# Kernel tuning notes

Measured on AMD Instinct MI355X. Metric: run time of the kernel, lower is better.

The kernel has to match this reference:

```python
import jax, jax.numpy as jnp
import numpy as np

I = 64    # input_size (per quaternion component)
H = 64    # hidden_size (per quaternion component)
T = 2048  # seq_len
B = 64    # batch
G = 3 * H # gate_size for QGRU


def hamilton_kernel(r, i, j, k):
    """Build the (4*In, 4*Out) real matrix of the quaternion (Hamilton) linear map,
    matching quaternion_linear: columns [r|i|j|k], each column a vstack of components."""
    return jnp.block([[r, i, j, k],
                      [-i, r, k, -j],
                      [-j, -k, r, i],
                      [-k, j, -i, r]])


def _gates(v, h):
    # v: (B, 4*3*h) laid out quaternion-major [r(3h)|i(3h)|j(3h)|k(3h)];
    # rearrange so each of the 3 gates is a contiguous quaternion vector (B, 4h).
    b = v.shape[0]
    return v.reshape(b, 4, 3, h).transpose(0, 2, 1, 3).reshape(b, 3, 4 * h)


def setup_inputs() -> dict:
    key = jax.random.key(0)
    ks = jax.random.split(key, 12)
    s_ih = 1.0 / np.sqrt(4 * I)
    s_hh = 1.0 / np.sqrt(4 * H)
    inp = {
        "x": jax.random.normal(ks[0], (T, B, 4 * I), dtype=jnp.float32),
        "hx": jnp.zeros((B, 4 * H), dtype=jnp.float32),
        "w_ih_r": jax.random.normal(ks[1], (I, G), dtype=jnp.float32) * s_ih,
        "w_ih_i": jax.random.normal(ks[2], (I, G), dtype=jnp.float32) * s_ih,
        "w_ih_j": jax.random.normal(ks[3], (I, G), dtype=jnp.float32) * s_ih,
        "w_ih_k": jax.random.normal(ks[4], (I, G), dtype=jnp.float32) * s_ih,
        "w_hh_r": jax.random.normal(ks[5], (H, G), dtype=jnp.float32) * s_hh,
        "w_hh_i": jax.random.normal(ks[6], (H, G), dtype=jnp.float32) * s_hh,
        "w_hh_j": jax.random.normal(ks[7], (H, G), dtype=jnp.float32) * s_hh,
        "w_hh_k": jax.random.normal(ks[8], (H, G), dtype=jnp.float32) * s_hh,
        "b_ih": jnp.zeros((4 * G,), dtype=jnp.float32),
        "b_hh": jnp.zeros((4 * G,), dtype=jnp.float32),
    }
    return inp


def reference(x, hx, w_ih_r, w_ih_i, w_ih_j, w_ih_k,
              w_hh_r, w_hh_i, w_hh_j, w_hh_k, b_ih, b_hh):
    h_sz = w_hh_r.shape[0]
    W_ih = hamilton_kernel(w_ih_r, w_ih_i, w_ih_j, w_ih_k)  # (4I, 4G)
    W_hh = hamilton_kernel(w_hh_r, w_hh_i, w_hh_j, w_hh_k)  # (4H, 4G)
    # Precompute all input-side gate preactivations in one big GEMM: (T,B,4G)
    gi = jnp.einsum('tbf,fg->tbg', x, W_ih) + b_ih

    def step(h, gi_t):
        gh = _gates(h @ W_hh + b_hh, h_sz)   # (B, 3, 4H)
        g = _gates(gi_t, h_sz)               # (B, 3, 4H)
        r = jax.nn.sigmoid(g[:, 0] + gh[:, 0])     # reset gate
        z = jax.nn.sigmoid(g[:, 1] + gh[:, 1])     # update (input) gate
        n = jnp.tanh(g[:, 2] + r * gh[:, 2])       # candidate
        h_new = n + z * (h - n)
        return h_new, h_new

    h_last, out = jax.lax.scan(step, hx, gi)
    return out, h_last
```

## Files before the change

kernel.cpp:

```cpp
#include <hip/hip_runtime.h>
#include <stdint.h>

#define T_SEQ 2048

typedef __attribute__((ext_vector_type(8))) short short8;
typedef __attribute__((ext_vector_type(4))) float f32x4;

__device__ __forceinline__ unsigned short f2bf(float f){
  unsigned int u = __float_as_uint(f);
  unsigned int r = u + 0x7fffu + ((u >> 16) & 1u);
  return (unsigned short)(r >> 16);
}
__device__ __forceinline__ float bf2f(unsigned short h){
  return __uint_as_float(((unsigned int)h) << 16);
}
__device__ __forceinline__ float sig_(float x){
  float e = __builtin_amdgcn_exp2f(-1.44269504089f * x);
  return __builtin_amdgcn_rcpf(1.0f + e);
}
__device__ __forceinline__ float tanh_(float x){
  float e = __builtin_amdgcn_exp2f(2.88539008178f * x);
  return 1.0f - 2.0f * __builtin_amdgcn_rcpf(1.0f + e);
}
__device__ __forceinline__ float ham_val(int qr, int qc, int kr, int nc,
    const float* wr, const float* wi, const float* wj, const float* wk){
  int cc = qr ^ qc;
  const float* w = (cc==0)?wr:(cc==1)?wi:(cc==2)?wj:wk;
  float v = w[kr*192 + nc];
  if ((0x5390u >> (qr*4+qc)) & 1u) v = -v;
  return v;
}

__global__ __launch_bounds__(256) void k_prep_bt(const float* __restrict__ wr,
    const float* __restrict__ wi, const float* __restrict__ wj,
    const float* __restrict__ wk, unsigned short* __restrict__ BT){
  int idx = blockIdx.x*256 + threadIdx.x;
  int c = idx / 768, kp = idx - c*768;
  int kk = kp & 255, piece = kp >> 8;
  int qr = kk >> 6, kr = kk & 63;
  int e = (c/48)*16 + (c & 15);
  int g = (c % 48) >> 4;
  int qc = e >> 6;
  int nc = g*64 + (e & 63);
  float v = ham_val(qr, qc, kr, nc, wr, wi, wj, wk);
  unsigned short hi = f2bf(v);
  unsigned short o = (piece == 1) ? f2bf(v - bf2f(hi)) : hi;
  BT[(size_t)c*768 + kp] = o;
}

__global__ __launch_bounds__(256) void k_prep_whh(const float* __restrict__ wr,
    const float* __restrict__ wi, const float* __restrict__ wj,
    const float* __restrict__ wk, unsigned short* __restrict__ WF){
  int idx = blockIdx.x*256 + threadIdx.x;
  int lane = idx & 63;
  int kt = (idx >> 6) & 1;
  int m  = (idx >> 7) & 3;
  int ws3 = idx >> 9;
  int w = ws3 / 3, s = ws3 - w*3;
  int quad = lane >> 4, u = lane & 15;
  int col = s*64 + w*16 + u;
  const float* mat = (m==0)?wr:(m==1)?wi:(m==2)?wj:wk;
  short8 o;
  #pragma unroll
  for (int j = 0; j < 8; j++){
    int k = kt*32 + quad*8 + j;
    o[j] = (short)f2bf(mat[k*192 + col]);
  }
  *(short8*)(WF + (size_t)idx*8) = o;
}

__global__ __launch_bounds__(256) void k_prep_bias(const float* __restrict__ bih,
    const float* __restrict__ bhh, float* __restrict__ bias){
  int c = blockIdx.x*256 + threadIdx.x;
  int e = (c/48)*16 + (c & 15);
  int g = (c % 48) >> 4;
  int n = (e >> 6)*192 + g*64 + (e & 63);
  bias[c] = bih[n] + bhh[n];
}

__global__ __launch_bounds__(256) void k_gemm_gi(const float* __restrict__ x,
    const unsigned short* __restrict__ BT, const float* __restrict__ bias,
    float* __restrict__ gi){
  __shared__ unsigned short As[128*64];
  __shared__ unsigned short Bs[128*64];
  int tid = threadIdx.x;
  int mb = blockIdx.x / 6, nb = blockIdx.x - mb*6;
  int lane = tid & 63, wid = tid >> 6;
  int quad = lane >> 4, u = lane & 15;
  int wvm = wid >> 1, wvn = wid & 1;
  int srow = tid >> 3, cb = tid & 7;
  f32x4 acc[4][4] = {};
  for (int kc = 0; kc < 12; kc++){
    bool lop = (kc >= 8);
    int kbase = (kc & 3) * 64;
    #pragma unroll
    for (int rd = 0; rd < 4; rd++){
      int m = rd*32 + srow;
      int lc = cb ^ (m & 7);
      const float* xp = x + (size_t)(mb*128 + m)*256 + kbase + lc*8;
      float4 v0 = *(const float4*)xp;
      float4 v1 = *(const float4*)(xp + 4);
      float vv[8] = {v0.x, v0.y, v0.z, v0.w, v1.x, v1.y, v1.z, v1.w};
      short8 ov;
      #pragma unroll
      for (int q = 0; q < 8; q++){
        unsigned short hi = f2bf(vv[q]);
        ov[q] = (short)(lop ? f2bf(vv[q] - bf2f(hi)) : hi);
      }
      *(short8*)&As[m*64 + cb*8] = ov;
    }
    #pragma unroll
    for (int rd = 0; rd < 4; rd++){
      int c = rd*32 + srow;
      int lc = cb ^ (c & 7);
      const unsigned short* bp = BT + (size_t)(nb*128 + c)*768 + kc*64 + lc*8;
      *(short8*)&Bs[c*64 + cb*8] = *(const short8*)bp;
    }
    __syncthreads();
    #pragma unroll
    for (int ks = 0; ks < 2; ks++){
      short8 af[4], bf[4];
      #pragma unroll
      for (int i=0;i<4;i++){
        int row = 64*wvm + 16*i + u;
        af[i] = *(const short8*)&As[row*64 + ((4*ks+quad) ^ (u & 7))*8];
      }
      #pragma unroll
      for (int j=0;j<4;j++){
        int row = 64*wvn + 16*j + u;
        bf[j] = *(const short8*)&Bs[row*64 + ((4*ks+quad) ^ (u & 7))*8];
      }
      #pragma unroll
      for (int i=0;i<4;i++)
        #pragma unroll
        for (int j=0;j<4;j++)
          acc[i][j] = __builtin_amdgcn_mfma_f32_16x16x32_bf16(af[i], bf[j], acc[i][j], 0, 0, 0);
    }
    __syncthreads();
  }
  int cb2 = nb*128 + 64*wvn;
  #pragma unroll
  for (int j=0;j<4;j++){
    float bj = bias[cb2 + 16*j + u];
    #pragma unroll
    for (int i=0;i<4;i++){
      float* gp = gi + (size_t)(mb*128 + 64*wvm + 16*i + quad*4)*768 + cb2 + 16*j + u;
      #pragma unroll
      for (int r=0;r<4;r++)
        gp[(size_t)r*768] = acc[i][j][r] + bj;
    }
  }
}

__global__ __launch_bounds__(256, 1) void k_rec(const float* __restrict__ gi,
    const short8* __restrict__ WF, const float* __restrict__ hx,
    float* __restrict__ out){
  __shared__ unsigned short hbuf[2][256];
  int tid = threadIdx.x;
  int b = blockIdx.x;
  int lane = tid & 63, w = tid >> 6;
  int quad = lane >> 4, u = lane & 15;
  short8 Bf[12][2];
  #pragma unroll
  for (int s = 0; s < 3; s++)
    #pragma unroll
    for (int m = 0; m < 4; m++)
      #pragma unroll
      for (int kt = 0; kt < 2; kt++)
        Bf[s*4+m][kt] = WF[(size_t)((((w*3+s)*4+m)*2+kt)*64 + lane)];
  int aoff = (((u & 3) ^ (u >> 2)) * 64) + quad*8;
  float sg1 = (quad & 1)              ?  1.f : -1.f;
  float sg2 = (quad==1 || quad==2)    ?  1.f : -1.f;
  float sg3 = (quad >> 1)             ?  1.f : -1.f;
  int e = quad*64 + w*16 + u;
  float h = hx[b*256 + e];
  hbuf[0][e] = f2bf(h);
  const float* gl = gi + (size_t)b*768 + (quad*4 + w)*48 + u;
  float* outp = out + (size_t)b*256 + e;
  float pf[4][3];
  #pragma unroll
  for (int j = 0; j < 4; j++){
    const float* p = gl + (size_t)j*49152;
    pf[j][0] = p[0]; pf[j][1] = p[16]; pf[j][2] = p[32];
  }
  const float* gp   = gl + (size_t)4*49152;
  const float* glast = gl + (size_t)(T_SEQ-1)*49152;
  asm volatile("s_waitcnt lgkmcnt(0)" ::: "memory");
  __builtin_amdgcn_s_barrier();
  asm volatile("" ::: "memory");
  for (int t0 = 0; t0 < T_SEQ; t0 += 4){
    #pragma unroll
    for (int j = 0; j < 4; j++){
      const unsigned short* hb = hbuf[j & 1];
      short8 a0 = *(const short8*)&hb[aoff];
      short8 a1 = *(const short8*)&hb[aoff + 32];
      f32x4 acc[12];
      #pragma unroll
      for (int sm = 0; sm < 12; sm++)
        acc[sm] = __builtin_amdgcn_mfma_f32_16x16x32_bf16(a0, Bf[sm][0],
                    (f32x4){0.f,0.f,0.f,0.f}, 0, 0, 0);
      #pragma unroll
      for (int sm = 0; sm < 12; sm++)
        acc[sm] = __builtin_amdgcn_mfma_f32_16x16x32_bf16(a1, Bf[sm][1],
                    acc[sm], 0, 0, 0);
      float o0 = acc[0][0] + sg1*acc[1][1] + sg2*acc[2][2]  + sg3*acc[3][3];
      float o1 = acc[4][0] + sg1*acc[5][1] + sg2*acc[6][2]  + sg3*acc[7][3];
      float o2 = acc[8][0] + sg1*acc[9][1] + sg2*acc[10][2] + sg3*acc[11][3];
      float r  = sig_(pf[j][0] + o0);
      float z  = sig_(pf[j][1] + o1);
      float nn = tanh_(pf[j][2] + r * o2);
      h = nn + z * (h - nn);
      int t = t0 + j;
      outp[(size_t)t * 16384] = h;
      hbuf[(j + 1) & 1][e] = f2bf(h);
      const float* pv = (gp <= glast) ? gp : glast;
      pf[j][0] = pv[0]; pf[j][1] = pv[16]; pf[j][2] = pv[32];
      gp += 49152;
      asm volatile("s_waitcnt lgkmcnt(0)" ::: "memory");
      __builtin_amdgcn_s_barrier();
      asm volatile("" ::: "memory");
    }
  }
  out[(size_t)T_SEQ * 16384 + b*256 + e] = h;
}

extern "C" void kernel_launch(void* const* d_in, const int* in_sizes, int n_in,
                              void* d_out, int out_size, void* d_ws, size_t ws_size,
                              hipStream_t stream){
  const float* x    = (const float*)d_in[0];
  const float* hx   = (const float*)d_in[1];
  const float* wihr = (const float*)d_in[2];
  const float* wihi = (const float*)d_in[3];
  const float* wihj = (const float*)d_in[4];
  const float* wihk = (const float*)d_in[5];
  const float* whhr = (const float*)d_in[6];
  const float* whhi = (const float*)d_in[7];
  const float* whhj = (const float*)d_in[8];
  const float* whhk = (const float*)d_in[9];
  const float* bih  = (const float*)d_in[10];
  const float* bhh  = (const float*)d_in[11];
  char* ws = (char*)d_ws;
  float* gi          = (float*)ws;
  unsigned short* BT = (unsigned short*)(ws + 402653184ull);
  unsigned short* WF = (unsigned short*)(ws + 403832832ull);
  float* bias        = (float*)(ws + 404226048ull);
  k_prep_bt  <<<dim3(2304), dim3(256), 0, stream>>>(wihr, wihi, wihj, wihk, BT);
  k_prep_whh <<<dim3(24),   dim3(256), 0, stream>>>(whhr, whhi, whhj, whhk, WF);
  k_prep_bias<<<dim3(3),    dim3(256), 0, stream>>>(bih, bhh, bias);
  k_gemm_gi  <<<dim3(6144), dim3(256), 0, stream>>>(x, BT, bias, gi);
  k_rec      <<<dim3(64),   dim3(256), 0, stream>>>(gi, (const short8*)WF, hx, (float*)d_out);
}
```

Baseline: 1.461 ms.

## Process two batch rows per recurrent block to interleave independent chains

The recurrent kernel now has each block advance two batch rows, A and B, at once. The MFMA chains and gate math for the two rows are interleaved, and both rows share a single barrier per timestep, so one row's latency can overlap the other's. The hidden-state LDS buffer is padded (stride 88) to reduce bank conflicts. In exchange only half as many blocks are launched, and each block does double the per-step work and uses more registers.

After: 1.998 ms. 1.37x slower.

```diff
diff --git a/kernel.cpp b/kernel.cpp
--- a/kernel.cpp
+++ b/kernel.cpp
@@ -155,9 +155,9 @@
 __global__ __launch_bounds__(256, 1) void k_rec(const float* __restrict__ gi,
     const short8* __restrict__ WF, const float* __restrict__ hx,
     float* __restrict__ out){
-  __shared__ unsigned short hbuf[2][256];
+  __shared__ unsigned short hbuf[2][2][4][88];
   int tid = threadIdx.x;
-  int b = blockIdx.x;
+  int b0 = blockIdx.x * 2;
   int lane = tid & 63, w = tid >> 6;
   int quad = lane >> 4, u = lane & 15;
   short8 Bf[12][2];
@@ -168,60 +168,99 @@
       #pragma unroll
       for (int kt = 0; kt < 2; kt++)
         Bf[s*4+m][kt] = WF[(size_t)((((w*3+s)*4+m)*2+kt)*64 + lane)];
-  int aoff = (((u & 3) ^ (u >> 2)) * 64) + quad*8;
+  int sg = (u & 3) ^ (u >> 2);
+  int abase = sg*88 + quad*8;
   float sg1 = (quad & 1)              ?  1.f : -1.f;
   float sg2 = (quad==1 || quad==2)    ?  1.f : -1.f;
   float sg3 = (quad >> 1)             ?  1.f : -1.f;
   int e = quad*64 + w*16 + u;
-  float h = hx[b*256 + e];
-  hbuf[0][e] = f2bf(h);
-  const float* gl = gi + (size_t)b*768 + (quad*4 + w)*48 + u;
-  float* outp = out + (size_t)b*256 + e;
-  float pf[4][3];
+  int wbase = quad*88 + w*16 + u;
+  unsigned short* hb = &hbuf[0][0][0][0];
+  float hA = hx[b0*256 + e];
+  float hB = hx[b0*256 + 256 + e];
+  hb[wbase]       = f2bf(hA);
+  hb[352 + wbase] = f2bf(hB);
+  const float* glA = gi + (size_t)b0*768 + (quad*4 + w)*48 + u;
+  const float* glB = glA + 768;
+  float* outA = out + (size_t)b0*256 + e;
+  float* outB = outA + 256;
+  float pfA[4][3], pfB[4][3];
   #pragma unroll
   for (int j = 0; j < 4; j++){
-    const float* p = gl + (size_t)j*49152;
-    pf[j][0] = p[0]; pf[j][1] = p[16]; pf[j][2] = p[32];
-  }
-  const float* gp   = gl + (size_t)4*49152;
-  const float* glast = gl + (size_t)(T_SEQ-1)*49152;
+    const float* pA = glA + (size_t)j*49152;
+    const float* pB = glB + (size_t)j*49152;
+    pfA[j][0]=pA[0]; pfA[j][1]=pA[16]; pfA[j][2]=pA[32];
+    pfB[j][0]=pB[0]; pfB[j][1]=pB[16]; pfB[j][2]=pB[32];
+  }
+  const float* gpA = glA + (size_t)4*49152;
+  const float* gpB = glB + (size_t)4*49152;
+  const float* glastA = glA + (size_t)(T_SEQ-1)*49152;
+  const float* glastB = glB + (size_t)(T_SEQ-1)*49152;
   asm volatile("s_waitcnt lgkmcnt(0)" ::: "memory");
   __builtin_amdgcn_s_barrier();
   asm volatile("" ::: "memory");
   for (int t0 = 0; t0 < T_SEQ; t0 += 4){
     #pragma unroll
     for (int j = 0; j < 4; j++){
-      const unsigned short* hb = hbuf[j & 1];
-      short8 a0 = *(const short8*)&hb[aoff];
-      short8 a1 = *(const short8*)&hb[aoff + 32];
-      f32x4 acc[12];
-      #pragma unroll
-      for (int sm = 0; sm < 12; sm++)
-        acc[sm] = __builtin_amdgcn_mfma_f32_16x16x32_bf16(a0, Bf[sm][0],
-                    (f32x4){0.f,0.f,0.f,0.f}, 0, 0, 0);
-      #pragma unroll
-      for (int sm = 0; sm < 12; sm++)
-        acc[sm] = __builtin_amdgcn_mfma_f32_16x16x32_bf16(a1, Bf[sm][1],
-                    acc[sm], 0, 0, 0);
-      float o0 = acc[0][0] + sg1*acc[1][1] + sg2*acc[2][2]  + sg3*acc[3][3];
-      float o1 = acc[4][0] + sg1*acc[5][1] + sg2*acc[6][2]  + sg3*acc[7][3];
-      float o2 = acc[8][0] + sg1*acc[9][1] + sg2*acc[10][2] + sg3*acc[11][3];
-      float r  = sig_(pf[j][0] + o0);
-      float z  = sig_(pf[j][1] + o1);
-      float nn = tanh_(pf[j][2] + r * o2);
-      h = nn + z * (h - nn);
+      int ph = j & 1;
+      const unsigned short* ha = hb + ph*704;
+      short8 a0A = *(const short8*)&ha[abase];
+      short8 a1A = *(const short8*)&ha[abase + 32];
+      short8 a0B = *(const short8*)&ha[352 + abase];
+      short8 a1B = *(const short8*)&ha[352 + abase + 32];
+      f32x4 accA[12], accB[12];
+      #pragma unroll
+      for (int sm = 0; sm < 12; sm++)
+        accA[sm] = __builtin_amdgcn_mfma_f32_16x16x32_bf16(a0A, Bf[sm][0],
+                     (f32x4){0.f,0.f,0.f,0.f}, 0, 0, 0);
+      #pragma unroll
+      for (int sm = 0; sm < 12; sm++)
+        accA[sm] = __builtin_amdgcn_mfma_f32_16x16x32_bf16(a1A, Bf[sm][1],
+                     accA[sm], 0, 0, 0);
+      #pragma unroll
+      for (int sm = 0; sm < 12; sm++)
+        accB[sm] = __builtin_amdgcn_mfma_f32_16x16x32_bf16(a0B, Bf[sm][0],
+                     (f32x4){0.f,0.f,0.f,0.f}, 0, 0, 0);
+      #pragma unroll
+      for (int sm = 0; sm < 12; sm++)
+        accB[sm] = __builtin_amdgcn_mfma_f32_16x16x32_bf16(a1B, Bf[sm][1],
+                     accB[sm], 0, 0, 0);
       int t = t0 + j;
-      outp[(size_t)t * 16384] = h;
-      hbuf[(j + 1) & 1][e] = f2bf(h);
-      const float* pv = (gp <= glast) ? gp : glast;
-      pf[j][0] = pv[0]; pf[j][1] = pv[16]; pf[j][2] = pv[32];
-      gp += 49152;
+      {
+        float o0 = accA[0][0] + sg1*accA[1][1] + sg2*accA[2][2]  + sg3*accA[3][3];
+        float o1 = accA[4][0] + sg1*accA[5][1] + sg2*accA[6][2]  + sg3*accA[7][3];
+        float o2 = accA[8][0] + sg1*accA[9][1] + sg2*accA[10][2] + sg3*accA[11][3];
+        float r  = sig_(pfA[j][0] + o0);
+        float z  = sig_(pfA[j][1] + o1);
+        float nn = tanh_(pfA[j][2] + r * o2);
+        hA = nn + z * (hA - nn);
+        outA[(size_t)t * 16384] = hA;
+        hb[(ph^1)*704 + wbase] = f2bf(hA);
+        const float* pv = (gpA <= glastA) ? gpA : glastA;
+        pfA[j][0] = pv[0]; pfA[j][1] = pv[16]; pfA[j][2] = pv[32];
+        gpA += 49152;
+      }
+      {
+        float o0 = accB[0][0] + sg1*accB[1][1] + sg2*accB[2][2]  + sg3*accB[3][3];
+        float o1 = accB[4][0] + sg1*accB[5][1] + sg2*accB[6][2]  + sg3*accB[7][3];
+        float o2 = accB[8][0] + sg1*accB[9][1] + sg2*accB[10][2] + sg3*accB[11][3];
+        float r  = sig_(pfB[j][0] + o0);
+        float z  = sig_(pfB[j][1] + o1);
+        float nn = tanh_(pfB[j][2] + r * o2);
+        hB = nn + z * (hB - nn);
+        outB[(size_t)t * 16384] = hB;
+        hb[(ph^1)*704 + 352 + wbase] = f2bf(hB);
+        const float* pv = (gpB <= glastB) ? gpB : glastB;
+        pfB[j][0] = pv[0]; pfB[j][1] = pv[16]; pfB[j][2] = pv[32];
+        gpB += 49152;
+      }
       asm volatile("s_waitcnt lgkmcnt(0)" ::: "memory");
       __builtin_amdgcn_s_barrier();
       asm volatile("" ::: "memory");
     }
   }
-  out[(size_t)T_SEQ * 16384 + b*256 + e] = h;
+  out[(size_t)T_SEQ * 16384 + b0*256 + e] = hA;
+  out[(size_t)T_SEQ * 16384 + b0*256 + 256 + e] = hB;
 }
 
 extern "C" void kernel_launch(void* const* d_in, const int* in_sizes, int n_in,
@@ -248,5 +287,5 @@
   k_prep_whh <<<dim3(24),   dim3(256), 0, stream>>>(whhr, whhi, whhj, whhk, WF);
   k_prep_bias<<<dim3(3),    dim3(256), 0, stream>>>(bih, bhh, bias);
   k_gemm_gi  <<<dim3(6144), dim3(256), 0, stream>>>(x, BT, bias, gi);
-  k_rec      <<<dim3(64),   dim3(256), 0, stream>>>(gi, (const short8*)WF, hx, (float*)d_out);
-}
+  k_rec      <<<dim3(32),   dim3(256), 0, stream>>>(gi, (const short8*)WF, hx, (float*)d_out);
+}
```

## Swizzle h LDS buffer, reorder MFMAs and defer output stores in recurrence

Applied to the files above, without the earlier changes.

Applies an XOR swizzle to the bf16 hidden-state LDS buffer so the A-fragment reads and the per-thread writes avoid bank conflicts. The output store for the previous step and the prefetch of gate inputs move to the top of each step so they sit off the critical path. The reset-gate MFMAs are issued first so its sigmoid can overlap the remaining MFMAs. The software bf16 rounding is replaced with the hardware v_cvt_pk_bf16_f32 instruction. Together these target the serial per-timestep latency, at the cost of more complex indexing and inline assembly.

New measurement: 1.518 ms. +3.9%, slower.

```diff
diff --git a/kernel.cpp b/kernel.cpp
--- a/kernel.cpp
+++ b/kernel.cpp
@@ -168,13 +168,16 @@
       #pragma unroll
       for (int kt = 0; kt < 2; kt++)
         Bf[s*4+m][kt] = WF[(size_t)((((w*3+s)*4+m)*2+kt)*64 + lane)];
-  int aoff = (((u & 3) ^ (u >> 2)) * 64) + quad*8;
+  int sg = (u & 3) ^ (u >> 2);
+  int a0off = sg*64 + ((quad ^ (2*sg)) & 7)*8;
+  int a1off = sg*64 + (((quad + 4) ^ (2*sg)) & 7)*8;
   float sg1 = (quad & 1)              ?  1.f : -1.f;
   float sg2 = (quad==1 || quad==2)    ?  1.f : -1.f;
   float sg3 = (quad >> 1)             ?  1.f : -1.f;
   int e = quad*64 + w*16 + u;
+  int wboff = quad*64 + (((w*2 + (u>>3)) ^ (2*quad)) & 7)*8 + (u & 7);
   float h = hx[b*256 + e];
-  hbuf[0][e] = f2bf(h);
+  hbuf[0][wboff] = f2bf(h);
   const float* gl = gi + (size_t)b*768 + (quad*4 + w)*48 + u;
   float* outp = out + (size_t)b*256 + e;
   float pf[4][3];
@@ -183,7 +186,7 @@
     const float* p = gl + (size_t)j*49152;
     pf[j][0] = p[0]; pf[j][1] = p[16]; pf[j][2] = p[32];
   }
-  const float* gp   = gl + (size_t)4*49152;
+  const float* gp    = gl + (size_t)4*49152;
   const float* glast = gl + (size_t)(T_SEQ-1)*49152;
   asm volatile("s_waitcnt lgkmcnt(0)" ::: "memory");
   __builtin_amdgcn_s_barrier();
@@ -191,36 +194,49 @@
   for (int t0 = 0; t0 < T_SEQ; t0 += 4){
     #pragma unroll
     for (int j = 0; j < 4; j++){
-      const unsigned short* hb = hbuf[j & 1];
-      short8 a0 = *(const short8*)&hb[aoff];
-      short8 a1 = *(const short8*)&hb[aoff + 32];
+      int ph = j & 1;
+      const unsigned short* hb = hbuf[ph];
+      short8 a0 = *(const short8*)&hb[a0off];
+      short8 a1 = *(const short8*)&hb[a1off];
+      if (t0 + j > 0)
+        outp[(size_t)(t0 + j - 1) * 16384] = h;
+      float g0 = pf[j][0], g1 = pf[j][1], g2 = pf[j][2];
+      const float* pv = (gp <= glast) ? gp : glast;
+      pf[j][0] = pv[0]; pf[j][1] = pv[16]; pf[j][2] = pv[32];
+      gp += 49152;
       f32x4 acc[12];
       #pragma unroll
-      for (int sm = 0; sm < 12; sm++)
+      for (int sm = 0; sm < 8; sm++)
         acc[sm] = __builtin_amdgcn_mfma_f32_16x16x32_bf16(a0, Bf[sm][0],
                     (f32x4){0.f,0.f,0.f,0.f}, 0, 0, 0);
       #pragma unroll
-      for (int sm = 0; sm < 12; sm++)
+      for (int sm = 0; sm < 8; sm++)
         acc[sm] = __builtin_amdgcn_mfma_f32_16x16x32_bf16(a1, Bf[sm][1],
                     acc[sm], 0, 0, 0);
       float o0 = acc[0][0] + sg1*acc[1][1] + sg2*acc[2][2]  + sg3*acc[3][3];
+      float r  = sig_(g0 + o0);
+      #pragma unroll
+      for (int sm = 8; sm < 12; sm++)
+        acc[sm] = __builtin_amdgcn_mfma_f32_16x16x32_bf16(a0, Bf[sm][0],
+                    (f32x4){0.f,0.f,0.f,0.f}, 0, 0, 0);
+      #pragma unroll
+      for (int sm = 8; sm < 12; sm++)
+        acc[sm] = __builtin_amdgcn_mfma_f32_16x16x32_bf16(a1, Bf[sm][1],
+                    acc[sm], 0, 0, 0);
       float o1 = acc[4][0] + sg1*acc[5][1] + sg2*acc[6][2]  + sg3*acc[7][3];
+      float z  = sig_(g1 + o1);
       float o2 = acc[8][0] + sg1*acc[9][1] + sg2*acc[10][2] + sg3*acc[11][3];
-      float r  = sig_(pf[j][0] + o0);
-      float z  = sig_(pf[j][1] + o1);
-      float nn = tanh_(pf[j][2] + r * o2);
+      float nn = tanh_(g2 + r * o2);
       h = nn + z * (h - nn);
-      int t = t0 + j;
-      outp[(size_t)t * 16384] = h;
-      hbuf[(j + 1) & 1][e] = f2bf(h);
-      const float* pv = (gp <= glast) ? gp : glast;
-      pf[j][0] = pv[0]; pf[j][1] = pv[16]; pf[j][2] = pv[32];
-      gp += 49152;
+      unsigned int hpk;
+      asm("v_cvt_pk_bf16_f32 %0, %1, %2" : "=v"(hpk) : "v"(h), "v"(h));
+      hbuf[ph ^ 1][wboff] = (unsigned short)hpk;
       asm volatile("s_waitcnt lgkmcnt(0)" ::: "memory");
       __builtin_amdgcn_s_barrier();
       asm volatile("" ::: "memory");
     }
   }
+  outp[(size_t)(T_SEQ - 1) * 16384] = h;
   out[(size_t)T_SEQ * 16384 + b*256 + e] = h;
 }
 
```
